# Kernel optimization log

Measured on AMD Instinct MI355X. Metric: run time of the kernel, lower is better.

The kernel has to match this reference:

```python
import jax, jax.numpy as jnp
import numpy as np

N = 50000      # num_nodes
DEG = 32       # fixed out-degree
E = N * DEG    # num graph edges
B = 1024       # num query edges (batch_size)
EPS = 1e-8
F_DROP = 0.7   # f_dropout used in random_fill


def _mlp(x, w1, b1, w2, b2):
    # Linear(1,d) -> ReLU -> Linear(d,1); x: [M,1]
    h = jax.nn.relu(x * w1[None, :] + b1[None, :])   # [M,d]
    return (h @ w2)[:, None] + b2                    # [M,1]


def setup_inputs() -> dict:
    key = jax.random.key(0)
    ks = jax.random.split(key, 20)
    inp = {
        'neighbors': jax.random.randint(ks[0], (N, DEG), 0, N, dtype=jnp.int32),
        'edge_w': jax.random.uniform(ks[1], (E,), dtype=jnp.float32),
        'src': jax.random.randint(ks[2], (B,), 0, N, dtype=jnp.int32),
        'dst': jax.random.randint(ks[3], (B,), 0, N, dtype=jnp.int32),
    }
    d = 64
    names = ['fe', 'fn', 'gp']
    i = 4
    for nm in names:
        s = 1.0 / np.sqrt(d)
        inp[nm + '_w1'] = jax.random.uniform(ks[i], (d,), minval=-1.0, maxval=1.0); i += 1
        inp[nm + '_b1'] = jax.random.uniform(ks[i], (d,), minval=-1.0, maxval=1.0); i += 1
        inp[nm + '_w2'] = jax.random.uniform(ks[i], (d,), minval=-s, maxval=s); i += 1
        inp[nm + '_b2'] = jax.random.uniform(ks[i], (1,), minval=-s, maxval=s); i += 1
    return inp


def reference(neighbors, edge_w, src, dst,
              fe_w1, fe_b1, fe_w2, fe_b2,
              fn_w1, fn_b1, fn_w2, fn_b2,
              gp_w1, gp_b1, gp_w2, gp_b2):
    # ---- node structural features: scatter_add of f_edge over edge dst ----
    cols = neighbors.reshape(-1)                                  # [E] edge dst (srcdst order)
    ew_A = _mlp(edge_w[:, None], fe_w1, fe_b1, fe_w2, fe_b2)      # [E,1]
    nsf = jnp.zeros((N, 1), dtype=ew_A.dtype).at[cols].add(ew_A)  # scatter_add -> [N,1]
    nsf = _mlp(nsf, fn_w1, fn_b1, fn_w2, fn_b2)                   # [N,1]
    nsf_v = nsf[:, 0]

    # ---- gather CSR rows for query src/dst; A.data == 1 (edge_w=False) ----
    row = jnp.repeat(jnp.arange(B, dtype=jnp.int32), DEG)         # [B*DEG]
    col_src = neighbors[src].reshape(-1)                          # [B*DEG]
    col_dst = neighbors[dst].reshape(-1)
    mat_src = jnp.zeros((B, N), dtype=nsf_v.dtype).at[row, col_src].add(nsf_v[col_src])
    mat_dst = jnp.zeros((B, N), dtype=nsf_v.dtype).at[row, col_dst].add(nsf_v[col_dst])

    # diag(mat_src @ mat_dst.T) == row-wise dot product (common neighbors)
    out_struct = jnp.sum(mat_src * mat_dst, axis=1)               # [B]

    # random_fill: add F.dropout(full(eps), p=f_dropout) -> eps/(1-p) w.p. (1-p)
    keep = 1.0 - F_DROP
    add_val = EPS / keep
    kd = jax.random.split(jax.random.key(42), 2)
    ms = mat_src + jax.random.bernoulli(kd[0], keep, (B, N)).astype(mat_src.dtype) * add_val
    md = mat_dst + jax.random.bernoulli(kd[1], keep, (B, N)).astype(mat_dst.dtype) * add_val
    D = jnp.linalg.norm(ms, axis=-1) * jnp.linalg.norm(md, axis=-1)  # [B]

    out_struct_n = _mlp((out_struct / D)[:, None], gp_w1, gp_b1, gp_w2, gp_b2)  # [B,1]
    return out_struct_n, nsf
```

## Files before the change

### kernel.cpp

```cpp
#include <hip/hip_runtime.h>

constexpr int NN   = 50000;
constexpr int KDEG = 32;
constexpr int NE   = NN * KDEG;
constexpr int NB   = 1024;
constexpr int NH   = 64;

constexpr int BINS = (NN + 255) >> 8;
constexpr int CAP  = 10240;
constexpr int EPB  = 2048;
constexpr int SCT_BLOCKS = (NE + EPB - 1) / EPB;

__device__ __forceinline__ float mlp64(float x,
                                       const float* __restrict__ w1,
                                       const float* __restrict__ b1,
                                       const float* __restrict__ w2,
                                       float b2) {
    float acc = 0.0f;
#pragma unroll 8
    for (int j = 0; j < NH; ++j) {
        float h = fmaxf(fmaf(x, w1[j], b1[j]), 0.0f);
        acc = fmaf(h, w2[j], acc);
    }
    return acc + b2;
}

__global__ __launch_bounds__(256) void scatter_kernel(
        const int* __restrict__ nbr, const float* __restrict__ ew,
        const float* __restrict__ w1, const float* __restrict__ b1,
        const float* __restrict__ w2, const float* __restrict__ b2p,
        uint2* __restrict__ sorted, int* __restrict__ alloc) {
    __shared__ uint2 stage[EPB];
    __shared__ int   hist[BINS];
    __shared__ int   lbase[BINS];
    __shared__ int   gbase[BINS];
    __shared__ int   scan[256];

    const int tid = threadIdx.x;
    for (int i = tid; i < BINS; i += 256) hist[i] = 0;
    __syncthreads();

    const int e0 = blockIdx.x * EPB;
    const float b2 = b2p[0];
    float val[8]; int node[8]; int loc[8];
#pragma unroll
    for (int j = 0; j < 8; ++j) {
        int e = e0 + tid + j * 256;
        if (e < NE) {
            node[j] = nbr[e];
            val[j]  = mlp64(ew[e], w1, b1, w2, b2);
            loc[j]  = atomicAdd(&hist[node[j] >> 8], 1);
        } else {
            node[j] = -1;
        }
    }
    __syncthreads();

    int v = (tid < BINS) ? hist[tid] : 0;
    scan[tid] = v;
    __syncthreads();
    for (int off = 1; off < 256; off <<= 1) {
        int t = (tid >= off) ? scan[tid - off] : 0;
        __syncthreads();
        scan[tid] += t;
        __syncthreads();
    }
    if (tid < BINS) lbase[tid] = scan[tid] - hist[tid];
    __syncthreads();

#pragma unroll
    for (int j = 0; j < 8; ++j) {
        if (node[j] >= 0) {
            int b = node[j] >> 8;
            stage[lbase[b] + loc[j]] = make_uint2(__float_as_uint(val[j]), (unsigned)node[j]);
        }
    }
    if (tid < BINS) {
        int c = hist[tid];
        gbase[tid] = c ? atomicAdd(&alloc[tid], c) : 0;
    }
    __syncthreads();

    const int total = lbase[BINS - 1] + hist[BINS - 1];
    for (int j = tid; j < total; j += 256) {
        uint2 p = stage[j];
        int b   = (int)(p.y >> 8);
        int dst = gbase[b] + (j - lbase[b]);
        if (dst < CAP) sorted[(size_t)b * CAP + dst] = p;
    }
}

__global__ __launch_bounds__(256) void reduce_kernel(
        const uint2* __restrict__ sorted, const int* __restrict__ alloc,
        const float* __restrict__ w1, const float* __restrict__ b1,
        const float* __restrict__ w2, const float* __restrict__ b2p,
        float* __restrict__ nsf) {
    __shared__ float acc[256];
    const int b = blockIdx.x, tid = threadIdx.x;
    acc[tid] = 0.0f;
    __syncthreads();
    const int cnt = min(alloc[b], CAP);
    const uint2* p = sorted + (size_t)b * CAP;
    for (int i = tid; i < cnt; i += 256) {
        uint2 e = p[i];
        atomicAdd(&acc[e.y & 255u], __uint_as_float(e.x));
    }
    __syncthreads();
    const int n = (b << 8) + tid;
    if (n < NN) nsf[n] = mlp64(acc[tid], w1, b1, w2, b2p[0]);
}

__global__ void edge_kernel(const int* __restrict__ nbr, const float* __restrict__ ew,
                            const float* __restrict__ w1, const float* __restrict__ b1,
                            const float* __restrict__ w2, const float* __restrict__ b2p,
                            float* __restrict__ nsf0) {
    int e = blockIdx.x * blockDim.x + threadIdx.x;
    if (e >= NE) return;
    float val = mlp64(ew[e], w1, b1, w2, b2p[0]);
    atomicAdd(&nsf0[nbr[e]], val);
}

__global__ void node_kernel(float* __restrict__ nsf,
                            const float* __restrict__ w1, const float* __restrict__ b1,
                            const float* __restrict__ w2, const float* __restrict__ b2p) {
    int n = blockIdx.x * blockDim.x + threadIdx.x;
    if (n >= NN) return;
    nsf[n] = mlp64(nsf[n], w1, b1, w2, b2p[0]);
}

__global__ void pair_kernel(const int* __restrict__ nbr,
                            const int* __restrict__ src, const int* __restrict__ dst,
                            const float* __restrict__ nsf,
                            const float* __restrict__ w1, const float* __restrict__ b1,
                            const float* __restrict__ w2, const float* __restrict__ b2p,
                            float* __restrict__ out) {
    int wave = (blockIdx.x * blockDim.x + threadIdx.x) >> 6;
    int lane = threadIdx.x & 63;
    if (wave >= NB) return;

    bool isSrc = lane < 32;
    int node = isSrc ? src[wave] : dst[wave];
    int id = nbr[node * KDEG + (lane & 31)];
    float v = nsf[id];

    int cntS = 0, cntD = 0;
#pragma unroll
    for (int k = 0; k < 32; ++k) {
        int o = __shfl(id, k, 64);
        cntS += (o == id) ? 1 : 0;
    }
#pragma unroll
    for (int k = 32; k < 64; ++k) {
        int o = __shfl(id, k, 64);
        cntD += (o == id) ? 1 : 0;
    }

    float v2 = v * v;
    float dotc = isSrc ? (float)cntD * v2 : 0.0f;
    float ns   = isSrc ? (float)cntS * v2 : 0.0f;
    float nd   = isSrc ? 0.0f : (float)cntD * v2;

#pragma unroll
    for (int off = 32; off > 0; off >>= 1) {
        dotc += __shfl_xor(dotc, off, 64);
        ns   += __shfl_xor(ns,   off, 64);
        nd   += __shfl_xor(nd,   off, 64);
    }

    if (lane == 0) {
        float D = sqrtf(ns) * sqrtf(nd);
        float x = dotc / fmaxf(D, 1e-30f);
        out[wave] = mlp64(x, w1, b1, w2, b2p[0]);
    }
}

extern "C" void kernel_launch(void* const* d_in, const int* in_sizes, int n_in,
                              void* d_out, int out_size, void* d_ws, size_t ws_size,
                              hipStream_t stream) {
    const int*   nbr    = (const int*)  d_in[0];
    const float* edge_w = (const float*)d_in[1];
    const int*   src    = (const int*)  d_in[2];
    const int*   dst    = (const int*)  d_in[3];
    const float* fe_w1  = (const float*)d_in[4];
    const float* fe_b1  = (const float*)d_in[5];
    const float* fe_w2  = (const float*)d_in[6];
    const float* fe_b2  = (const float*)d_in[7];
    const float* fn_w1  = (const float*)d_in[8];
    const float* fn_b1  = (const float*)d_in[9];
    const float* fn_w2  = (const float*)d_in[10];
    const float* fn_b2  = (const float*)d_in[11];
    const float* gp_w1  = (const float*)d_in[12];
    const float* gp_b1  = (const float*)d_in[13];
    const float* gp_w2  = (const float*)d_in[14];
    const float* gp_b2  = (const float*)d_in[15];

    float* out = (float*)d_out;
    float* nsf = (float*)d_out + NB;

    const size_t sorted_bytes = (size_t)BINS * CAP * sizeof(uint2);
    const size_t need = sorted_bytes + BINS * sizeof(int);

    if (ws_size >= need) {
        uint2* sorted = (uint2*)d_ws;
        int*   alloc  = (int*)((char*)d_ws + sorted_bytes);
        hipMemsetAsync(alloc, 0, BINS * sizeof(int), stream);
        scatter_kernel<<<SCT_BLOCKS, 256, 0, stream>>>(nbr, edge_w,
                                                       fe_w1, fe_b1, fe_w2, fe_b2,
                                                       sorted, alloc);
        reduce_kernel<<<BINS, 256, 0, stream>>>(sorted, alloc,
                                                fn_w1, fn_b1, fn_w2, fn_b2, nsf);
    } else {
        hipMemsetAsync(nsf, 0, (size_t)NN * sizeof(float), stream);
        edge_kernel<<<NE / 256, 256, 0, stream>>>(nbr, edge_w, fe_w1, fe_b1, fe_w2, fe_b2, nsf);
        node_kernel<<<(NN + 255) / 256, 256, 0, stream>>>(nsf, fn_w1, fn_b1, fn_w2, fn_b2);
    }

    pair_kernel<<<(NB * 64) / 256, 256, 0, stream>>>(nbr, src, dst, nsf,
                                                     gp_w1, gp_b1, gp_w2, gp_b2, out);
}
```

Measured before the change: 138.2 us.

## Split sorted buffer into float values and byte offsets, use wave-shuffle scan

The intermediate bucket-sorted edge buffer changes from 8-byte (value,node) pairs to a float array plus a one-byte low-node index, with 16-bit node ids in shared staging. This cuts global write and read traffic for the 1.6M edge records. The block-wide shared-memory prefix scan with many barriers becomes a single-wave shuffle scan over 4 bins per lane, and the global slot allocation moves before the staging writes. The reduce kernel uses 512 threads per bin to raise parallelism for the shared atomic accumulation. Byte-wide global stores are less efficient per element than wide stores.

```diff
diff --git a/kernel.cpp b/kernel.cpp
--- a/kernel.cpp
+++ b/kernel.cpp
@@ -29,12 +29,13 @@
         const int* __restrict__ nbr, const float* __restrict__ ew,
         const float* __restrict__ w1, const float* __restrict__ b1,
         const float* __restrict__ w2, const float* __restrict__ b2p,
-        uint2* __restrict__ sorted, int* __restrict__ alloc) {
-    __shared__ uint2 stage[EPB];
-    __shared__ int   hist[BINS];
-    __shared__ int   lbase[BINS];
-    __shared__ int   gbase[BINS];
-    __shared__ int   scan[256];
+        float* __restrict__ sortedV, unsigned char* __restrict__ sortedB,
+        int* __restrict__ alloc) {
+    __shared__ float          sV[EPB];
+    __shared__ unsigned short sN[EPB];
+    __shared__ int hist[BINS];
+    __shared__ int lbase[BINS + 1];
+    __shared__ int gbase[BINS];
 
     const int tid = threadIdx.x;
     for (int i = tid; i < BINS; i += 256) hist[i] = 0;
@@ -56,58 +57,77 @@
     }
     __syncthreads();
 
-    int v = (tid < BINS) ? hist[tid] : 0;
-    scan[tid] = v;
-    __syncthreads();
-    for (int off = 1; off < 256; off <<= 1) {
-        int t = (tid >= off) ? scan[tid - off] : 0;
-        __syncthreads();
-        scan[tid] += t;
-        __syncthreads();
-    }
-    if (tid < BINS) lbase[tid] = scan[tid] - hist[tid];
-    __syncthreads();
+    if (tid < 64) {
+        int b0 = tid * 4;
+        int c0 = (b0 + 0 < BINS) ? hist[b0 + 0] : 0;
+        int c1 = (b0 + 1 < BINS) ? hist[b0 + 1] : 0;
+        int c2 = (b0 + 2 < BINS) ? hist[b0 + 2] : 0;
+        int c3 = (b0 + 3 < BINS) ? hist[b0 + 3] : 0;
+        int s = c0 + c1 + c2 + c3;
+        int p = s;
+#pragma unroll
+        for (int off = 1; off < 64; off <<= 1) {
+            int t = __shfl_up(p, off, 64);
+            if (tid >= off) p += t;
+        }
+        int excl = p - s;
+        if (b0 + 0 < BINS) lbase[b0 + 0] = excl;
+        if (b0 + 1 < BINS) lbase[b0 + 1] = excl + c0;
+        if (b0 + 2 < BINS) lbase[b0 + 2] = excl + c0 + c1;
+        if (b0 + 3 < BINS) lbase[b0 + 3] = excl + c0 + c1 + c2;
+        if (tid == 63) lbase[BINS] = p;
+    }
+    __syncthreads();
+
+    if (tid < BINS) {
+        int c = hist[tid];
+        gbase[tid] = c ? atomicAdd(&alloc[tid], c) : 0;
+    }
 
 #pragma unroll
     for (int j = 0; j < 8; ++j) {
         if (node[j] >= 0) {
             int b = node[j] >> 8;
-            stage[lbase[b] + loc[j]] = make_uint2(__float_as_uint(val[j]), (unsigned)node[j]);
-        }
-    }
-    if (tid < BINS) {
-        int c = hist[tid];
-        gbase[tid] = c ? atomicAdd(&alloc[tid], c) : 0;
-    }
-    __syncthreads();
-
-    const int total = lbase[BINS - 1] + hist[BINS - 1];
+            int p = lbase[b] + loc[j];
+            sV[p] = val[j];
+            sN[p] = (unsigned short)node[j];
+        }
+    }
+    __syncthreads();
+
+    const int total = lbase[BINS];
     for (int j = tid; j < total; j += 256) {
-        uint2 p = stage[j];
-        int b   = (int)(p.y >> 8);
+        int n   = sN[j];
+        int b   = n >> 8;
         int dst = gbase[b] + (j - lbase[b]);
-        if (dst < CAP) sorted[(size_t)b * CAP + dst] = p;
-    }
-}
-
-__global__ __launch_bounds__(256) void reduce_kernel(
-        const uint2* __restrict__ sorted, const int* __restrict__ alloc,
+        if (dst < CAP) {
+            sortedV[(size_t)b * CAP + dst] = sV[j];
+            sortedB[(size_t)b * CAP + dst] = (unsigned char)(n & 255);
+        }
+    }
+}
+
+__global__ __launch_bounds__(512) void reduce_kernel(
+        const float* __restrict__ sortedV, const unsigned char* __restrict__ sortedB,
+        const int* __restrict__ alloc,
         const float* __restrict__ w1, const float* __restrict__ b1,
         const float* __restrict__ w2, const float* __restrict__ b2p,
         float* __restrict__ nsf) {
     __shared__ float acc[256];
     const int b = blockIdx.x, tid = threadIdx.x;
-    acc[tid] = 0.0f;
+    if (tid < 256) acc[tid] = 0.0f;
     __syncthreads();
     const int cnt = min(alloc[b], CAP);
-    const uint2* p = sorted + (size_t)b * CAP;
-    for (int i = tid; i < cnt; i += 256) {
-        uint2 e = p[i];
-        atomicAdd(&acc[e.y & 255u], __uint_as_float(e.x));
-    }
-    __syncthreads();
-    const int n = (b << 8) + tid;
-    if (n < NN) nsf[n] = mlp64(acc[tid], w1, b1, w2, b2p[0]);
+    const float* pv = sortedV + (size_t)b * CAP;
+    const unsigned char* pb = sortedB + (size_t)b * CAP;
+    for (int i = tid; i < cnt; i += 512) {
+        atomicAdd(&acc[pb[i]], pv[i]);
+    }
+    __syncthreads();
+    if (tid < 256) {
+        const int n = (b << 8) + tid;
+        if (n < NN) nsf[n] = mlp64(acc[tid], w1, b1, w2, b2p[0]);
+    }
 }
 
 __global__ void edge_kernel(const int* __restrict__ nbr, const float* __restrict__ ew,
@@ -197,17 +217,20 @@
     float* out = (float*)d_out;
     float* nsf = (float*)d_out + NB;
 
-    const size_t sorted_bytes = (size_t)BINS * CAP * sizeof(uint2);
-    const size_t need = sorted_bytes + BINS * sizeof(int);
+    const size_t nEnt    = (size_t)BINS * CAP;
+    const size_t v_bytes = nEnt * sizeof(float);
+    const size_t b_bytes = (nEnt + 255) & ~(size_t)255;
+    const size_t need    = v_bytes + b_bytes + BINS * sizeof(int);
 
     if (ws_size >= need) {
-        uint2* sorted = (uint2*)d_ws;
-        int*   alloc  = (int*)((char*)d_ws + sorted_bytes);
+        float*         sortedV = (float*)d_ws;
+        unsigned char* sortedB = (unsigned char*)d_ws + v_bytes;
+        int*           alloc   = (int*)((char*)d_ws + v_bytes + b_bytes);
         hipMemsetAsync(alloc, 0, BINS * sizeof(int), stream);
         scatter_kernel<<<SCT_BLOCKS, 256, 0, stream>>>(nbr, edge_w,
                                                        fe_w1, fe_b1, fe_w2, fe_b2,
-                                                       sorted, alloc);
-        reduce_kernel<<<BINS, 256, 0, stream>>>(sorted, alloc,
+                                                       sortedV, sortedB, alloc);
+        reduce_kernel<<<BINS, 512, 0, stream>>>(sortedV, sortedB, alloc,
                                                 fn_w1, fn_b1, fn_w2, fn_b2, nsf);
     } else {
         hipMemsetAsync(nsf, 0, (size_t)NN * sizeof(float), stream);
```

Result: no change. 137.8 us (-0.3%).
